# Kernel optimization log

Hardware: AMD Instinct MI355X
Metric: run time of the kernel (lower is better)

The kernel has to match this reference:

```python
import jax, jax.numpy as jnp
import numpy as np

B, SQ, SK, D, UNITS = 4, 2048, 2048, 1024, 1024

def setup_inputs() -> dict:
    key = jax.random.key(0)
    ks = jax.random.split(key, 5)
    scale = 1.0 / np.sqrt(D)
    return {
        "q": jax.random.normal(ks[0], (B, SQ, D), dtype=jnp.float32),
        "k": jax.random.normal(ks[1], (B, SK, D), dtype=jnp.float32),
        "v": jax.random.normal(ks[2], (B, SK, D), dtype=jnp.float32),
        "W1_w": jax.random.normal(ks[3], (D, UNITS), dtype=jnp.float32) * scale,
        "W1_b": jnp.zeros((UNITS,), dtype=jnp.float32),
        "W2_w": jax.random.normal(ks[4], (D, UNITS), dtype=jnp.float32) * scale,
        "W2_b": jnp.zeros((UNITS,), dtype=jnp.float32),
    }

def reference(q, k, v, W1_w, W1_b, W2_w, W2_b):
    # Dense projections (keras Dense: x @ W + b)
    l1 = q @ W1_w + W1_b            # [B, Sq, units]
    l2 = k @ W2_w + W2_b            # [B, Sk, units]
    # score = l1 @ l2^T, scaled by sqrt(score.shape[2]) == sqrt(Sk) (as in original)
    inv_scale = 1.0 / np.sqrt(k.shape[1]).astype(np.float32)
    score = jnp.einsum('bqu,bku->bqk', l1, l2) * inv_scale  # [B, Sq, Sk]
    dist = jax.nn.softmax(score, axis=-1)
    att = jnp.einsum('bqk,bkd->bqd', dist, v)               # [B, Sq, d_v]
    return att
```

## Files before the change

kernel.cpp:

```cpp
#include <hip/hip_runtime.h>
#include <cmath>
#include <stdint.h>


typedef short short8 __attribute__((ext_vector_type(8)));
typedef float f32x4 __attribute__((ext_vector_type(4)));
typedef __bf16 bf16x8 __attribute__((ext_vector_type(8)));

typedef __attribute__((address_space(3))) void lds_void;
typedef __attribute__((address_space(1))) void gbl_void;

__device__ __forceinline__ unsigned short f2b(float x) {
    unsigned u = __builtin_bit_cast(unsigned, x);
    u += 0x7fffu + ((u >> 16) & 1u);
    return (unsigned short)(u >> 16);
}
__device__ __forceinline__ float b2f(unsigned short x) {
    unsigned u = ((unsigned)x) << 16;
    return __builtin_bit_cast(float, u);
}

__global__ void cast2_kernel(const float* __restrict__ in0,
                             const float* __restrict__ in1,
                             unsigned short* __restrict__ out0,
                             unsigned short* __restrict__ out1) {
    const float* in = blockIdx.y ? in1 : in0;
    unsigned short* out = blockIdx.y ? out1 : out0;
    long i = ((long)blockIdx.x * blockDim.x + threadIdx.x) * 8;
    float4 a = *(const float4*)(in + i);
    float4 b = *(const float4*)(in + i + 4);
    union { short8 v; unsigned short u[8]; } r;
    r.u[0] = f2b(a.x); r.u[1] = f2b(a.y); r.u[2] = f2b(a.z); r.u[3] = f2b(a.w);
    r.u[4] = f2b(b.x); r.u[5] = f2b(b.y); r.u[6] = f2b(b.z); r.u[7] = f2b(b.w);
    *(short8*)(out + i) = r.v;
}

__global__ void transpose_cast_kernel(const float* __restrict__ in,
                                      unsigned short* __restrict__ out,
                                      int R, int C) {
    __shared__ float tile[32][33];
    in  += (long)blockIdx.z * R * C;
    out += (long)blockIdx.z * R * C;
    const int t = threadIdx.x;
    const int rt = blockIdx.x * 32, ct = blockIdx.y * 32;
    {
        int r = t >> 3, c4 = (t & 7) * 4;
        float4 a = *(const float4*)(in + (long)(rt + r) * C + ct + c4);
        tile[r][c4 + 0] = a.x; tile[r][c4 + 1] = a.y;
        tile[r][c4 + 2] = a.z; tile[r][c4 + 3] = a.w;
    }
    __syncthreads();
    {
        int c = t >> 3, rg = (t & 7) * 4;
        ushort4 o;
        o.x = f2b(tile[rg + 0][c]); o.y = f2b(tile[rg + 1][c]);
        o.z = f2b(tile[rg + 2][c]); o.w = f2b(tile[rg + 3][c]);
        *(ushort4*)(out + (long)(ct + c) * R + rt + rg) = o;
    }
}

__global__ void transpose_cast2_kernel(const float* __restrict__ inA,
                                       const float* __restrict__ inB,
                                       unsigned short* __restrict__ outA,
                                       unsigned short* __restrict__ outB,
                                       int R, int C) {
    __shared__ float tile[32][33];
    const float* in = blockIdx.z ? inB : inA;
    unsigned short* out = blockIdx.z ? outB : outA;
    const int t = threadIdx.x;
    const int rt = blockIdx.x * 32, ct = blockIdx.y * 32;
    {
        int r = t >> 3, c4 = (t & 7) * 4;
        float4 a = *(const float4*)(in + (long)(rt + r) * C + ct + c4);
        tile[r][c4 + 0] = a.x; tile[r][c4 + 1] = a.y;
        tile[r][c4 + 2] = a.z; tile[r][c4 + 3] = a.w;
    }
    __syncthreads();
    {
        int c = t >> 3, rg = (t & 7) * 4;
        ushort4 o;
        o.x = f2b(tile[rg + 0][c]); o.y = f2b(tile[rg + 1][c]);
        o.z = f2b(tile[rg + 2][c]); o.w = f2b(tile[rg + 3][c]);
        *(ushort4*)(out + (long)(ct + c) * R + rt + rg) = o;
    }
}

__device__ __forceinline__ void load16_to_lds(const unsigned short* g,
                                              unsigned short* l) {
    __builtin_amdgcn_global_load_lds((gbl_void*)g, (lds_void*)l, 16, 0, 0);
}

template <int OUT_BF16>
__global__ void gemm_bt_kernel(const unsigned short* __restrict__ A,
                               const unsigned short* __restrict__ Bt,
                               const float* __restrict__ bias,
                               void* __restrict__ Cout,
                               int M, int N, int K,
                               float scale, int hasBias,
                               long sA, long sB, long sC) {
    __shared__ __align__(16) unsigned short As[128 * 32];
    __shared__ __align__(16) unsigned short Bs[128 * 32];

    int bx, by, bz;
    {
        const int nx = gridDim.x;
        const int Rt = gridDim.y * gridDim.z;
        if ((Rt & 7) == 0) {
            int flat = ((int)blockIdx.z * gridDim.y + blockIdx.y) * nx + blockIdx.x;
            int rpx = Rt >> 3;
            int c = flat & 7;
            int j = flat >> 3;
            bx = j / rpx;
            int yg = c * rpx + (j - bx * rpx);
            bz = yg / gridDim.y;
            by = yg - bz * gridDim.y;
        } else {
            bx = blockIdx.x; by = blockIdx.y; bz = blockIdx.z;
        }
    }

    A  += (long)bz * sA;
    Bt += (long)bz * sB;

    const int t = threadIdx.x;
    const int lane = t & 63;
    const int wave = t >> 6;
    const int wm = wave >> 1, wn = wave & 1;
    const int row0 = by * 128;
    const int col0 = bx * 128;

    const int rowS = t >> 2;
    const int sw   = (rowS >> 1) & 3;
    const int kcS  = ((t & 3) ^ sw) * 8;
    const unsigned short* gA0 = A  + (long)(row0 + rowS) * K + kcS;
    const unsigned short* gA1 = A  + (long)(row0 + rowS + 64) * K + kcS;
    const unsigned short* gB0 = Bt + (long)(col0 + rowS) * K + kcS;
    const unsigned short* gB1 = Bt + (long)(col0 + rowS + 64) * K + kcS;
    unsigned short* lA0 = As + wave * 512;
    unsigned short* lA1 = As + wave * 512 + 2048;
    unsigned short* lB0 = Bs + wave * 512;
    unsigned short* lB1 = Bs + wave * 512 + 2048;

    const int lr = lane & 15;
    const int quad = lane >> 4;
    const int pcA = (quad ^ ((lr >> 1) & 3)) * 8;

    f32x4 acc[4][4];
#pragma unroll
    for (int i = 0; i < 4; i++)
#pragma unroll
        for (int j = 0; j < 4; j++) acc[i][j] = f32x4{0.f, 0.f, 0.f, 0.f};

    for (int k0 = 0; k0 < K; k0 += 32) {
        load16_to_lds(gA0 + k0, lA0);
        load16_to_lds(gA1 + k0, lA1);
        load16_to_lds(gB0 + k0, lB0);
        load16_to_lds(gB1 + k0, lB1);
        __syncthreads();

        bf16x8 a[4], b[4];
#pragma unroll
        for (int i = 0; i < 4; i++) {
            a[i] = __builtin_bit_cast(bf16x8,
                *(const short8*)(As + (wm * 64 + i * 16 + lr) * 32 + pcA));
            b[i] = __builtin_bit_cast(bf16x8,
                *(const short8*)(Bs + (wn * 64 + i * 16 + lr) * 32 + pcA));
        }
#pragma unroll
        for (int i = 0; i < 4; i++)
#pragma unroll
            for (int j = 0; j < 4; j++)
                acc[i][j] = __builtin_amdgcn_mfma_f32_16x16x32_bf16(
                    a[i], b[j], acc[i][j], 0, 0, 0);
        __syncthreads();
    }

    const long cbase = (long)bz * sC;
#pragma unroll
    for (int j = 0; j < 4; j++) {
        const int gcol = col0 + wn * 64 + j * 16 + lr;
        const float bv = hasBias ? bias[gcol] : 0.0f;
#pragma unroll
        for (int i = 0; i < 4; i++) {
            const int growb = row0 + wm * 64 + i * 16 + quad * 4;
#pragma unroll
            for (int r = 0; r < 4; r++) {
                float val = acc[i][j][r] * scale + bv;
                long off = cbase + (long)(growb + r) * N + gcol;
                if (OUT_BF16) ((unsigned short*)Cout)[off] = f2b(val);
                else          ((float*)Cout)[off] = val;
            }
        }
    }
}

__global__ void softmax_kernel(unsigned short* __restrict__ s) {
    __shared__ float wmax[4], wsum[4];
    const int t = threadIdx.x;
    const long base = (long)blockIdx.x * 2048 + t * 8;
    union { short8 v; unsigned short u[8]; } raw;
    raw.v = *(const short8*)(s + base);
    float x[8];
#pragma unroll
    for (int i = 0; i < 8; i++) x[i] = b2f(raw.u[i]);
    float m = x[0];
#pragma unroll
    for (int i = 1; i < 8; i++) m = fmaxf(m, x[i]);
#pragma unroll
    for (int off = 32; off; off >>= 1) m = fmaxf(m, __shfl_xor(m, off));
    if ((t & 63) == 0) wmax[t >> 6] = m;
    __syncthreads();
    m = fmaxf(fmaxf(wmax[0], wmax[1]), fmaxf(wmax[2], wmax[3]));
    float p[8], sum = 0.f;
#pragma unroll
    for (int i = 0; i < 8; i++) { p[i] = __expf(x[i] - m); sum += p[i]; }
#pragma unroll
    for (int off = 32; off; off >>= 1) sum += __shfl_xor(sum, off);
    if ((t & 63) == 0) wsum[t >> 6] = sum;
    __syncthreads();
    sum = wsum[0] + wsum[1] + wsum[2] + wsum[3];
    const float inv = 1.0f / sum;
#pragma unroll
    for (int i = 0; i < 8; i++) raw.u[i] = f2b(p[i] * inv);
    *(short8*)(s + base) = raw.v;
}

extern "C" void kernel_launch(void* const* d_in, const int* in_sizes, int n_in,
                              void* d_out, int out_size, void* d_ws, size_t ws_size,
                              hipStream_t stream) {
    const float* q   = (const float*)d_in[0];
    const float* k   = (const float*)d_in[1];
    const float* v   = (const float*)d_in[2];
    const float* W1w = (const float*)d_in[3];
    const float* W1b = (const float*)d_in[4];
    const float* W2w = (const float*)d_in[5];
    const float* W2b = (const float*)d_in[6];
    float* out = (float*)d_out;

    const int B = 4, SQ = 2048, SK = 2048, D = 1024, U = 1024;
    char* ws = (char*)d_ws;
    const size_t MB = 1024 * 1024;
    unsigned short* qbf = (unsigned short*)(ws + 0);
    unsigned short* kbf = (unsigned short*)(ws + 16 * MB);
    unsigned short* vT  = (unsigned short*)(ws + 32 * MB);
    unsigned short* W1t = (unsigned short*)(ws + 48 * MB);
    unsigned short* W2t = (unsigned short*)(ws + 50 * MB);
    unsigned short* l1  = (unsigned short*)(ws + 52 * MB);
    unsigned short* l2  = (unsigned short*)(ws + 68 * MB);
    unsigned short* sc  = (unsigned short*)(ws + 0);

    cast2_kernel<<<dim3((B * SQ * D) / (256 * 8), 2), 256, 0, stream>>>(
        q, k, qbf, kbf);
    transpose_cast2_kernel<<<dim3(D / 32, U / 32, 2), 256, 0, stream>>>(
        W1w, W2w, W1t, W2t, D, U);
    transpose_cast_kernel<<<dim3(SK / 32, D / 32, B), 256, 0, stream>>>(v, vT, SK, D);
    gemm_bt_kernel<1><<<dim3(U / 128, (B * SQ) / 128, 1), 256, 0, stream>>>(
        qbf, W1t, W1b, l1, B * SQ, U, D, 1.0f, 1, 0, 0, 0);
    gemm_bt_kernel<1><<<dim3(U / 128, (B * SK) / 128, 1), 256, 0, stream>>>(
        kbf, W2t, W2b, l2, B * SK, U, D, 1.0f, 1, 0, 0, 0);
    const float invs = 1.0f / sqrtf((float)SK);
    gemm_bt_kernel<1><<<dim3(SK / 128, SQ / 128, B), 256, 0, stream>>>(
        l1, l2, nullptr, sc, SQ, SK, U, invs, 0,
        (long)SQ * U, (long)SK * U, (long)SQ * SK);
    softmax_kernel<<<B * SQ, 256, 0, stream>>>(sc);
    gemm_bt_kernel<0><<<dim3(D / 128, SQ / 128, B), 256, 0, stream>>>(
        sc, vT, nullptr, out, SQ, D, SK, 1.0f, 0,
        (long)SQ * SK, (long)D * SK, (long)SQ * D);
}
```

Before: 313.2 us.

## Double GEMM K-tile to 64, merge projection GEMMs and transpose launches

```diff
diff --git a/kernel.cpp b/kernel.cpp
--- a/kernel.cpp
+++ b/kernel.cpp
@@ -35,12 +35,27 @@
     *(short8*)(out + i) = r.v;
 }
 
-__global__ void transpose_cast_kernel(const float* __restrict__ in,
-                                      unsigned short* __restrict__ out,
-                                      int R, int C) {
+__global__ void prep_transpose_kernel(const float* __restrict__ v,
+                                      const float* __restrict__ W1,
+                                      const float* __restrict__ W2,
+                                      unsigned short* __restrict__ vT,
+                                      unsigned short* __restrict__ W1t,
+                                      unsigned short* __restrict__ W2t) {
     __shared__ float tile[32][33];
-    in  += (long)blockIdx.z * R * C;
-    out += (long)blockIdx.z * R * C;
+    const int bz = blockIdx.z;
+    const float* in;
+    unsigned short* out;
+    int R, C;
+    if (bz < 4) {
+        R = 2048; C = 1024;
+        in = v + (long)bz * R * C;
+        out = vT + (long)bz * R * C;
+    } else {
+        R = 1024; C = 1024;
+        if (blockIdx.x >= 32) return;
+        in = (bz == 4) ? W1 : W2;
+        out = (bz == 4) ? W1t : W2t;
+    }
     const int t = threadIdx.x;
     const int rt = blockIdx.x * 32, ct = blockIdx.y * 32;
     {
@@ -59,32 +74,6 @@
     }
 }
 
-__global__ void transpose_cast2_kernel(const float* __restrict__ inA,
-                                       const float* __restrict__ inB,
-                                       unsigned short* __restrict__ outA,
-                                       unsigned short* __restrict__ outB,
-                                       int R, int C) {
-    __shared__ float tile[32][33];
-    const float* in = blockIdx.z ? inB : inA;
-    unsigned short* out = blockIdx.z ? outB : outA;
-    const int t = threadIdx.x;
-    const int rt = blockIdx.x * 32, ct = blockIdx.y * 32;
-    {
-        int r = t >> 3, c4 = (t & 7) * 4;
-        float4 a = *(const float4*)(in + (long)(rt + r) * C + ct + c4);
-        tile[r][c4 + 0] = a.x; tile[r][c4 + 1] = a.y;
-        tile[r][c4 + 2] = a.z; tile[r][c4 + 3] = a.w;
-    }
-    __syncthreads();
-    {
-        int c = t >> 3, rg = (t & 7) * 4;
-        ushort4 o;
-        o.x = f2b(tile[rg + 0][c]); o.y = f2b(tile[rg + 1][c]);
-        o.z = f2b(tile[rg + 2][c]); o.w = f2b(tile[rg + 3][c]);
-        *(ushort4*)(out + (long)(ct + c) * R + rt + rg) = o;
-    }
-}
-
 __device__ __forceinline__ void load16_to_lds(const unsigned short* g,
                                               unsigned short* l) {
     __builtin_amdgcn_global_load_lds((gbl_void*)g, (lds_void*)l, 16, 0, 0);
@@ -93,13 +82,14 @@
 template <int OUT_BF16>
 __global__ void gemm_bt_kernel(const unsigned short* __restrict__ A,
                                const unsigned short* __restrict__ Bt,
-                               const float* __restrict__ bias,
+                               const float* __restrict__ bias0,
+                               const float* __restrict__ bias1,
                                void* __restrict__ Cout,
                                int M, int N, int K,
                                float scale, int hasBias,
                                long sA, long sB, long sC) {
-    __shared__ __align__(16) unsigned short As[128 * 32];
-    __shared__ __align__(16) unsigned short Bs[128 * 32];
+    __shared__ __align__(16) unsigned short As[128 * 64];
+    __shared__ __align__(16) unsigned short Bs[128 * 64];
 
     int bx, by, bz;
     {
@@ -129,21 +119,26 @@
     const int row0 = by * 128;
     const int col0 = bx * 128;
 
-    const int rowS = t >> 2;
-    const int sw   = (rowS >> 1) & 3;
-    const int kcS  = ((t & 3) ^ sw) * 8;
-    const unsigned short* gA0 = A  + (long)(row0 + rowS) * K + kcS;
-    const unsigned short* gA1 = A  + (long)(row0 + rowS + 64) * K + kcS;
-    const unsigned short* gB0 = Bt + (long)(col0 + rowS) * K + kcS;
-    const unsigned short* gB1 = Bt + (long)(col0 + rowS + 64) * K + kcS;
-    unsigned short* lA0 = As + wave * 512;
-    unsigned short* lA1 = As + wave * 512 + 2048;
-    unsigned short* lB0 = Bs + wave * 512;
-    unsigned short* lB1 = Bs + wave * 512 + 2048;
+    const int rS = lane >> 3;
+    const int kOffS = ((lane & 7) ^ rS) * 8;
+    const unsigned short* gA[4];
+    const unsigned short* gB[4];
+    unsigned short* lA[4];
+    unsigned short* lB[4];
+#pragma unroll
+    for (int i = 0; i < 4; i++) {
+        const int rowl = i * 32 + wave * 8 + rS;
+        const int ldsrow = i * 32 + wave * 8;
+        gA[i] = A  + (long)(row0 + rowl) * K + kOffS;
+        gB[i] = Bt + (long)(col0 + rowl) * K + kOffS;
+        lA[i] = As + ldsrow * 64;
+        lB[i] = Bs + ldsrow * 64;
+    }
 
     const int lr = lane & 15;
     const int quad = lane >> 4;
-    const int pcA = (quad ^ ((lr >> 1) & 3)) * 8;
+    const int pc0 = (quad ^ (lr & 7)) * 8;
+    const int pc1 = ((4 + quad) ^ (lr & 7)) * 8;
 
     f32x4 acc[4][4];
 #pragma unroll
@@ -151,35 +146,41 @@
 #pragma unroll
         for (int j = 0; j < 4; j++) acc[i][j] = f32x4{0.f, 0.f, 0.f, 0.f};
 
-    for (int k0 = 0; k0 < K; k0 += 32) {
-        load16_to_lds(gA0 + k0, lA0);
-        load16_to_lds(gA1 + k0, lA1);
-        load16_to_lds(gB0 + k0, lB0);
-        load16_to_lds(gB1 + k0, lB1);
+    for (int k0 = 0; k0 < K; k0 += 64) {
+#pragma unroll
+        for (int i = 0; i < 4; i++) {
+            load16_to_lds(gA[i] + k0, lA[i]);
+            load16_to_lds(gB[i] + k0, lB[i]);
+        }
         __syncthreads();
 
-        bf16x8 a[4], b[4];
-#pragma unroll
-        for (int i = 0; i < 4; i++) {
-            a[i] = __builtin_bit_cast(bf16x8,
-                *(const short8*)(As + (wm * 64 + i * 16 + lr) * 32 + pcA));
-            b[i] = __builtin_bit_cast(bf16x8,
-                *(const short8*)(Bs + (wn * 64 + i * 16 + lr) * 32 + pcA));
-        }
-#pragma unroll
-        for (int i = 0; i < 4; i++)
-#pragma unroll
-            for (int j = 0; j < 4; j++)
-                acc[i][j] = __builtin_amdgcn_mfma_f32_16x16x32_bf16(
-                    a[i], b[j], acc[i][j], 0, 0, 0);
+#pragma unroll
+        for (int ks = 0; ks < 2; ks++) {
+            const int pc = ks ? pc1 : pc0;
+            bf16x8 a[4], b[4];
+#pragma unroll
+            for (int i = 0; i < 4; i++) {
+                a[i] = __builtin_bit_cast(bf16x8,
+                    *(const short8*)(As + (wm * 64 + i * 16 + lr) * 64 + pc));
+                b[i] = __builtin_bit_cast(bf16x8,
+                    *(const short8*)(Bs + (wn * 64 + i * 16 + lr) * 64 + pc));
+            }
+#pragma unroll
+            for (int i = 0; i < 4; i++)
+#pragma unroll
+                for (int j = 0; j < 4; j++)
+                    acc[i][j] = __builtin_amdgcn_mfma_f32_16x16x32_bf16(
+                        a[i], b[j], acc[i][j], 0, 0, 0);
+        }
         __syncthreads();
     }
 
+    const float* bp = (bz && bias1) ? bias1 : bias0;
     const long cbase = (long)bz * sC;
 #pragma unroll
     for (int j = 0; j < 4; j++) {
         const int gcol = col0 + wn * 64 + j * 16 + lr;
-        const float bv = hasBias ? bias[gcol] : 0.0f;
+        const float bv = hasBias ? bp[gcol] : 0.0f;
 #pragma unroll
         for (int i = 0; i < 4; i++) {
             const int growb = row0 + wm * 64 + i * 16 + quad * 4;
@@ -251,19 +252,17 @@
 
     cast2_kernel<<<dim3((B * SQ * D) / (256 * 8), 2), 256, 0, stream>>>(
         q, k, qbf, kbf);
-    transpose_cast2_kernel<<<dim3(D / 32, U / 32, 2), 256, 0, stream>>>(
-        W1w, W2w, W1t, W2t, D, U);
-    transpose_cast_kernel<<<dim3(SK / 32, D / 32, B), 256, 0, stream>>>(v, vT, SK, D);
-    gemm_bt_kernel<1><<<dim3(U / 128, (B * SQ) / 128, 1), 256, 0, stream>>>(
-        qbf, W1t, W1b, l1, B * SQ, U, D, 1.0f, 1, 0, 0, 0);
-    gemm_bt_kernel<1><<<dim3(U / 128, (B * SK) / 128, 1), 256, 0, stream>>>(
-        kbf, W2t, W2b, l2, B * SK, U, D, 1.0f, 1, 0, 0, 0);
+    prep_transpose_kernel<<<dim3(SK / 32, D / 32, 6), 256, 0, stream>>>(
+        v, W1w, W2w, vT, W1t, W2t);
+    gemm_bt_kernel<1><<<dim3(U / 128, (B * SQ) / 128, 2), 256, 0, stream>>>(
+        qbf, W1t, W1b, W2b, l1, B * SQ, U, D, 1.0f, 1,
+        (long)8 * 1024 * 1024, (long)1024 * 1024, (long)8 * 1024 * 1024);
     const float invs = 1.0f / sqrtf((float)SK);
     gemm_bt_kernel<1><<<dim3(SK / 128, SQ / 128, B), 256, 0, stream>>>(
-        l1, l2, nullptr, sc, SQ, SK, U, invs, 0,
+        l1, l2, nullptr, nullptr, sc, SQ, SK, U, invs, 0,
         (long)SQ * U, (long)SK * U, (long)SQ * SK);
     softmax_kernel<<<B * SQ, 256, 0, stream>>>(sc);
     gemm_bt_kernel<0><<<dim3(D / 128, SQ / 128, B), 256, 0, stream>>>(
-        sc, vT, nullptr, out, SQ, D, SK, 1.0f, 0,
+        sc, vT, nullptr, nullptr, out, SQ, D, SK, 1.0f, 0,
         (long)SQ * SK, (long)D * SK, (long)SQ * D);
 }
```

Result: faster. 283.9 us (-9.4%).
